# Kernel tuning notes

Measured on AMD Instinct MI355X. Metric: run time of the kernel, lower is better.

## Reference

```python
import jax, jax.numpy as jnp
import numpy as np

B, S, D_MODEL = 4, 1024, 1024
HEADS, D_KEY, D_VAL = 16, 64, 64


def setup_inputs() -> dict:
    key = jax.random.key(0)
    ks = jax.random.split(key, 8)
    # glorot-ish scaled params
    sk = 1.0 / np.sqrt(D_MODEL)
    X = jax.random.normal(ks[0], (B, S, D_MODEL), dtype=jnp.float32)
    Wk = jax.random.normal(ks[1], (HEADS, D_MODEL, D_KEY), dtype=jnp.float32) * sk
    Wq = jax.random.normal(ks[2], (HEADS, D_MODEL, D_KEY), dtype=jnp.float32) * sk
    Wv = jax.random.normal(ks[3], (HEADS, D_MODEL, D_VAL), dtype=jnp.float32) * sk
    bk = jnp.zeros((HEADS, D_KEY), dtype=jnp.float32)
    bq = jnp.zeros((HEADS, D_KEY), dtype=jnp.float32)
    bv = jnp.zeros((HEADS, D_VAL), dtype=jnp.float32)
    Wo = jax.random.normal(ks[4], (HEADS * D_VAL, D_MODEL), dtype=jnp.float32) * (1.0 / np.sqrt(HEADS * D_VAL))
    bo = jnp.zeros((D_MODEL,), dtype=jnp.float32)
    return {"X": X, "Wk": Wk, "bk": bk, "Wq": Wq, "bq": bq, "Wv": Wv, "bv": bv, "Wo": Wo, "bo": bo}


def reference(X, Wk, bk, Wq, bq, Wv, bv, Wo, bo):
    # Per-head projections, batched over heads (original loops in Python)
    K = jnp.einsum('bsd,hdk->bhsk', X, Wk) + bk[None, :, None, :]
    Q = jnp.einsum('bsd,hdk->bhsk', X, Wq) + bq[None, :, None, :]
    V = jnp.einsum('bsd,hdv->bhsv', X, Wv) + bv[None, :, None, :]
    d_k = K.shape[-1]
    scores = jnp.einsum('bhqk,bhsk->bhqs', Q, K) / jnp.sqrt(jnp.asarray(d_k, X.dtype))
    A = jax.nn.softmax(scores, axis=-1)           # [B,H,S,S]
    Z = jnp.einsum('bhqs,bhsv->bhqv', A, V)        # [B,H,S,Dv]
    # concat heads: [B,S,H*Dv]
    Zc = jnp.transpose(Z, (0, 2, 1, 3)).reshape(X.shape[0], X.shape[1], -1)
    # output projection + residual; dropout is identity at inference
    return Zc @ Wo + bo + X
```

## Files before the change

kernel.cpp:

```cpp
#include <hip/hip_runtime.h>
#include <hip/hip_bf16.h>

typedef __bf16 bf16x8 __attribute__((ext_vector_type(8)));
typedef float f32x4 __attribute__((ext_vector_type(4)));
typedef unsigned short u16;
typedef u16 u16x4 __attribute__((ext_vector_type(4)));
typedef u16 u16x8 __attribute__((ext_vector_type(8)));

#define LDA 72

__device__ inline u16 f2bf(float f) {
    union { float f; unsigned u; } v; v.f = f;
    unsigned r = v.u + 0x7fffu + ((v.u >> 16) & 1u);
    return (u16)(r >> 16);
}

#define GLD16(g, l) __builtin_amdgcn_global_load_lds( \
    (const __attribute__((address_space(1))) unsigned int*)(g), \
    (__attribute__((address_space(3))) unsigned int*)(l), 16, 0, 0)

__global__ void k_prep(const float* __restrict__ X, u16* __restrict__ Xb,
                       const float* __restrict__ Wk, const float* __restrict__ Wq,
                       const float* __restrict__ Wv, u16* __restrict__ WT,
                       const float* __restrict__ Wo, u16* __restrict__ WoT) {
    __shared__ u16 Ls[64 * LDA];
    int bid = blockIdx.x, t = threadIdx.x;
    if (bid < 4096) {
        int idx = bid * 256 + t;
        float4 v = *(const float4*)&X[(size_t)idx * 4];
        u16x4 o; o.x = f2bf(v.x); o.y = f2bf(v.y); o.z = f2bf(v.z); o.w = f2bf(v.w);
        *(u16x4*)&Xb[(size_t)idx * 4] = o;
        return;
    }
    if (bid < 4864) {
        int b2 = bid - 4096;
        int dt = b2 & 15, h = (b2 >> 4) & 15, p = b2 >> 8;
        const float* src = (p == 0 ? Wk : p == 1 ? Wq : Wv);
        int r0 = t >> 4, c4 = t & 15;
        for (int j = 0; j < 4; j++) {
            int d = r0 + j * 16;
            float4 v = *(const float4*)&src[((size_t)h * 1024 + dt * 64 + d) * 64 + c4 * 4];
            u16* q = &Ls[d * LDA + c4 * 4];
            q[0] = f2bf(v.x); q[1] = f2bf(v.y); q[2] = f2bf(v.z); q[3] = f2bf(v.w);
        }
        __syncthreads();
        int nk = t >> 2, cd = t & 3;
        u16 tmp[16];
        for (int j = 0; j < 16; j++) tmp[j] = Ls[(cd * 16 + j) * LDA + nk];
        size_t o = ((size_t)(p * 1024 + h * 64 + nk)) * 1024 + dt * 64 + cd * 16;
        *(u16x8*)&WT[o] = *(u16x8*)&tmp[0];
        *(u16x8*)&WT[o + 8] = *(u16x8*)&tmp[8];
        return;
    }
    {
        int b2 = bid - 4864;
        int dt = b2 & 15, nt2 = b2 >> 4;
        int r0 = t >> 4, c4 = t & 15;
        for (int j = 0; j < 4; j++) {
            int d = r0 + j * 16;
            float4 v = *(const float4*)&Wo[(size_t)(dt * 64 + d) * 1024 + nt2 * 64 + c4 * 4];
            u16* q = &Ls[d * LDA + c4 * 4];
            q[0] = f2bf(v.x); q[1] = f2bf(v.y); q[2] = f2bf(v.z); q[3] = f2bf(v.w);
        }
        __syncthreads();
        int nr = t >> 2, cd = t & 3;
        u16 tmp[16];
        for (int j = 0; j < 16; j++) tmp[j] = Ls[(cd * 16 + j) * LDA + nr];
        size_t o = ((size_t)(nt2 * 64 + nr)) * 1024 + dt * 64 + cd * 16;
        *(u16x8*)&WoT[o] = *(u16x8*)&tmp[0];
        *(u16x8*)&WoT[o + 8] = *(u16x8*)&tmp[8];
    }
}

__global__ __launch_bounds__(256) void k_qkv(
    const u16* __restrict__ Xb, const u16* __restrict__ WT,
    const float* __restrict__ bk, const float* __restrict__ bq, const float* __restrict__ bv,
    u16* __restrict__ Kw, u16* __restrict__ Qw, u16* __restrict__ Vtw)
{
    __shared__ u16 As[128 * 64];
    __shared__ u16 Bs[128 * 64];
    int tid = threadIdx.x, w = tid >> 6, lane = tid & 63, quad = lane >> 4, l16 = lane & 15;
    int wm = w & 1, wn = w >> 1;
    int m0 = blockIdx.x * 128, n0 = blockIdx.y * 128;
    int rl = lane >> 3, ch = lane & 7;
    int swch = ch ^ rl;
    const u16* Ag = Xb + (size_t)(m0 + w * 32 + rl) * 1024 + swch * 8;
    const u16* Bg = WT + (size_t)(n0 + w * 32 + rl) * 1024 + swch * 8;

    f32x4 acc[4][4] = {};
    for (int k0 = 0; k0 < 1024; k0 += 64) {
        for (int i = 0; i < 4; i++) {
            GLD16(Ag + (size_t)i * 8 * 1024 + k0, &As[(w * 32 + i * 8) * 64]);
            GLD16(Bg + (size_t)i * 8 * 1024 + k0, &Bs[(w * 32 + i * 8) * 64]);
        }
        __syncthreads();
        for (int ks = 0; ks < 2; ks++) {
            bf16x8 af[4], bf[4];
            int c = (ks << 2) | quad;
            for (int mt = 0; mt < 4; mt++) {
                int row = wm * 64 + mt * 16 + l16;
                af[mt] = *(bf16x8*)&As[row * 64 + (c ^ (row & 7)) * 8];
            }
            for (int nt = 0; nt < 4; nt++) {
                int row = wn * 64 + nt * 16 + l16;
                bf[nt] = *(bf16x8*)&Bs[row * 64 + (c ^ (row & 7)) * 8];
            }
            for (int mt = 0; mt < 4; mt++)
                for (int nt = 0; nt < 4; nt++)
                    acc[mt][nt] = __builtin_amdgcn_mfma_f32_16x16x32_bf16(af[mt], bf[nt], acc[mt][nt], 0, 0, 0);
        }
        __syncthreads();
    }
    int hb = blockIdx.y * 2 + wn;
    int p = hb >> 4, hh = hb & 15;
    const float* bias = (p == 0 ? bk : p == 1 ? bq : bv) + hh * 64;
    if (p < 2) {
        u16* dst = (p == 0) ? Kw : Qw;
        float sc = (p == 0) ? 0.125f : 1.0f;
        for (int mt = 0; mt < 4; mt++)
            for (int nt = 0; nt < 4; nt++) {
                int nk = nt * 16 + l16;
                float bb = bias[nk];
                for (int r = 0; r < 4; r++) {
                    int m = m0 + wm * 64 + mt * 16 + quad * 4 + r;
                    int b = m >> 10, s = m & 1023;
                    dst[((size_t)((b << 4) + hh) * 1024 + s) * 64 + nk] = f2bf((acc[mt][nt][r] + bb) * sc);
                }
            }
    } else {
        for (int mt = 0; mt < 4; mt++)
            for (int nt = 0; nt < 4; nt++) {
                int nk = nt * 16 + l16;
                float bb = bias[nk];
                int mb = m0 + wm * 64 + mt * 16 + quad * 4;
                int b = mb >> 10, s = mb & 1023;
                u16x4 o;
                for (int r = 0; r < 4; r++) o[r] = f2bf(acc[mt][nt][r] + bb);
                *(u16x4*)&Vtw[((size_t)((b << 4) + hh) * 64 + nk) * 1024 + s] = o;
            }
    }
}

__global__ __launch_bounds__(256) void k_attn(
    const u16* __restrict__ Qw, const u16* __restrict__ Kw,
    const u16* __restrict__ Vtw, u16* __restrict__ Zw)
{
    __shared__ u16 Ks[2][64 * 64];
    __shared__ u16 Vs[2][64 * 64];
    __shared__ u16 Ps[4 * 2 * 16 * LDA];
    int tid = threadIdx.x, w = tid >> 6, lane = tid & 63, quad = lane >> 4, l16 = lane & 15;
    int bh = blockIdx.x, q0 = blockIdx.y * 128;
    const u16* Qp = Qw + (size_t)bh * 65536;
    int rl = lane >> 3, ch = lane & 7, swch = ch ^ rl;
    const u16* Kg = Kw + (size_t)bh * 65536 + (w * 16 + rl) * 64 + swch * 8;
    const u16* Vg = Vtw + (size_t)bh * 65536 + (size_t)(w * 16 + rl) * 1024 + swch * 8;

    bf16x8 aq[2][2];
    for (int g = 0; g < 2; g++)
        for (int ks = 0; ks < 2; ks++)
            aq[g][ks] = *(const bf16x8*)&Qp[(size_t)(q0 + w * 32 + g * 16 + l16) * 64 + ks * 32 + quad * 8];

    f32x4 acc[2][4] = {};
    f32x4 accs[2] = {};
    __bf16 onev = (__bf16)1.0f;
    bf16x8 ones = {onev, onev, onev, onev, onev, onev, onev, onev};
    u16* Pw0 = Ps + (w * 2) * 16 * LDA;
    u16* Pw1 = Pw0 + 16 * LDA;

#define STAGE(st, buf) { int s0_ = (st) * 64; \
    for (int i = 0; i < 2; i++) { \
        GLD16(Kg + (s0_ + i * 8) * 64, &Ks[buf][(w * 16 + i * 8) * 64]); \
        GLD16(Vg + (size_t)i * 8 * 1024 + s0_, &Vs[buf][(w * 16 + i * 8) * 64]); } }

    STAGE(0, 0);
    for (int st = 0; st < 16; st++) {
        int buf = st & 1;
        __syncthreads();
        if (st < 15) STAGE(st + 1, buf ^ 1);
        f32x4 sacc[2][4] = {};
        for (int ks = 0; ks < 2; ks++) {
            int c = (ks << 2) | quad;
            for (int nt = 0; nt < 4; nt++) {
                int row = nt * 16 + l16;
                bf16x8 kf = *(bf16x8*)&Ks[buf][row * 64 + (c ^ (row & 7)) * 8];
                sacc[0][nt] = __builtin_amdgcn_mfma_f32_16x16x32_bf16(aq[0][ks], kf, sacc[0][nt], 0, 0, 0);
                sacc[1][nt] = __builtin_amdgcn_mfma_f32_16x16x32_bf16(aq[1][ks], kf, sacc[1][nt], 0, 0, 0);
            }
        }
        for (int g = 0; g < 2; g++) {
            u16* Pw = g ? Pw1 : Pw0;
            for (int nt = 0; nt < 4; nt++)
                for (int r = 0; r < 4; r++) {
                    float p = __builtin_exp2f(__builtin_fmaf(sacc[g][nt][r], 1.44269504f, -23.0831206f));
                    union { float f; unsigned u; } cv; cv.f = p;
                    Pw[(quad * 4 + r) * LDA + nt * 16 + l16] = (u16)((cv.u + 0x8000u) >> 16);
                }
        }
        for (int ks2 = 0; ks2 < 2; ks2++) {
            int c = (ks2 << 2) | quad;
            bf16x8 ap0 = *(bf16x8*)&Pw0[l16 * LDA + ks2 * 32 + quad * 8];
            bf16x8 ap1 = *(bf16x8*)&Pw1[l16 * LDA + ks2 * 32 + quad * 8];
            accs[0] = __builtin_amdgcn_mfma_f32_16x16x32_bf16(ap0, ones, accs[0], 0, 0, 0);
            accs[1] = __builtin_amdgcn_mfma_f32_16x16x32_bf16(ap1, ones, accs[1], 0, 0, 0);
            for (int ntv = 0; ntv < 4; ntv++) {
                int row = ntv * 16 + l16;
                bf16x8 vf = *(bf16x8*)&Vs[buf][row * 64 + (c ^ (row & 7)) * 8];
                acc[0][ntv] = __builtin_amdgcn_mfma_f32_16x16x32_bf16(ap0, vf, acc[0][ntv], 0, 0, 0);
                acc[1][ntv] = __builtin_amdgcn_mfma_f32_16x16x32_bf16(ap1, vf, acc[1][ntv], 0, 0, 0);
            }
        }
    }
#undef STAGE
    int b = bh >> 4, h = bh & 15;
    for (int g = 0; g < 2; g++)
        for (int r = 0; r < 4; r++) {
            float inv = 1.f / accs[g][r];
            int q = q0 + w * 32 + g * 16 + quad * 4 + r;
            for (int ntv = 0; ntv < 4; ntv++)
                Zw[((size_t)(b * 1024 + q)) * 1024 + h * 64 + ntv * 16 + l16] = f2bf(acc[g][ntv][r] * inv);
        }
}

__global__ __launch_bounds__(256) void k_oproj(
    const u16* __restrict__ Zw, const u16* __restrict__ WoT, const float* __restrict__ bo,
    const float* __restrict__ X, float* __restrict__ out)
{
    __shared__ u16 As[128 * 64];
    __shared__ u16 Bs[128 * 64];
    int tid = threadIdx.x, w = tid >> 6, lane = tid & 63, quad = lane >> 4, l16 = lane & 15;
    int wm = w & 1, wn = w >> 1;
    int m0 = blockIdx.x * 128, n0 = blockIdx.y * 128;
    int rl = lane >> 3, ch = lane & 7;
    int swch = ch ^ rl;
    const u16* Ag = Zw + (size_t)(m0 + w * 32 + rl) * 1024 + swch * 8;
    const u16* Bg = WoT + (size_t)(n0 + w * 32 + rl) * 1024 + swch * 8;

    f32x4 acc[4][4] = {};
    for (int k0 = 0; k0 < 1024; k0 += 64) {
        for (int i = 0; i < 4; i++) {
            GLD16(Ag + (size_t)i * 8 * 1024 + k0, &As[(w * 32 + i * 8) * 64]);
            GLD16(Bg + (size_t)i * 8 * 1024 + k0, &Bs[(w * 32 + i * 8) * 64]);
        }
        __syncthreads();
        for (int ks = 0; ks < 2; ks++) {
            bf16x8 af[4], bf[4];
            int c = (ks << 2) | quad;
            for (int mt = 0; mt < 4; mt++) {
                int row = wm * 64 + mt * 16 + l16;
                af[mt] = *(bf16x8*)&As[row * 64 + (c ^ (row & 7)) * 8];
            }
            for (int nt = 0; nt < 4; nt++) {
                int row = wn * 64 + nt * 16 + l16;
                bf[nt] = *(bf16x8*)&Bs[row * 64 + (c ^ (row & 7)) * 8];
            }
            for (int mt = 0; mt < 4; mt++)
                for (int nt = 0; nt < 4; nt++)
                    acc[mt][nt] = __builtin_amdgcn_mfma_f32_16x16x32_bf16(af[mt], bf[nt], acc[mt][nt], 0, 0, 0);
        }
        __syncthreads();
    }
    for (int mt = 0; mt < 4; mt++)
        for (int nt = 0; nt < 4; nt++) {
            int n = n0 + wn * 64 + nt * 16 + l16;
            float bb = bo[n];
            for (int r = 0; r < 4; r++) {
                int m = m0 + wm * 64 + mt * 16 + quad * 4 + r;
                out[(size_t)m * 1024 + n] = acc[mt][nt][r] + bb + X[(size_t)m * 1024 + n];
            }
        }
}

extern "C" void kernel_launch(void* const* d_in, const int* in_sizes, int n_in,
                              void* d_out, int out_size, void* d_ws, size_t ws_size,
                              hipStream_t stream) {
    const float* X  = (const float*)d_in[0];
    const float* Wk = (const float*)d_in[1];
    const float* bk = (const float*)d_in[2];
    const float* Wq = (const float*)d_in[3];
    const float* bq = (const float*)d_in[4];
    const float* Wv = (const float*)d_in[5];
    const float* bv = (const float*)d_in[6];
    const float* Wo = (const float*)d_in[7];
    const float* bo = (const float*)d_in[8];
    u16* ws = (u16*)d_ws;
    const size_t NQ = 4u * 16u * 1024u * 64u;
    u16* Qw  = ws;
    u16* Kw  = ws + NQ;
    u16* Vtw = ws + 2 * NQ;
    u16* Zw  = ws + 3 * NQ;
    u16* WT  = ws + 4 * NQ;
    u16* WoT = WT + 3 * 1048576;
    u16* Xb  = WoT + 1048576;
    float* outp = (float*)d_out;

    k_prep <<<5120, 256, 0, stream>>>(X, Xb, Wk, Wq, Wv, WT, Wo, WoT);
    k_qkv  <<<dim3(32, 24), 256, 0, stream>>>(Xb, WT, bk, bq, bv, Kw, Qw, Vtw);
    k_attn <<<dim3(64, 8), 256, 0, stream>>>(Qw, Kw, Vtw, Zw);
    k_oproj<<<dim3(32, 8), 256, 0, stream>>>(Zw, WoT, bo, X, outp);
}
```

Measured before the change: 187.6 us.

## Fuse all four stages into one persistent cooperative kernel with grid syncs

```diff
diff --git a/kernel.cpp b/kernel.cpp
--- a/kernel.cpp
+++ b/kernel.cpp
@@ -1,5 +1,8 @@
 #include <hip/hip_runtime.h>
 #include <hip/hip_bf16.h>
+#include <hip/hip_cooperative_groups.h>
+
+namespace cg = cooperative_groups;
 
 typedef __bf16 bf16x8 __attribute__((ext_vector_type(8)));
 typedef float f32x4 __attribute__((ext_vector_type(4)));
@@ -19,24 +22,21 @@
     (const __attribute__((address_space(1))) unsigned int*)(g), \
     (__attribute__((address_space(3))) unsigned int*)(l), 16, 0, 0)
 
-__global__ void k_prep(const float* __restrict__ X, u16* __restrict__ Xb,
-                       const float* __restrict__ Wk, const float* __restrict__ Wq,
-                       const float* __restrict__ Wv, u16* __restrict__ WT,
-                       const float* __restrict__ Wo, u16* __restrict__ WoT) {
-    __shared__ u16 Ls[64 * LDA];
-    int bid = blockIdx.x, t = threadIdx.x;
-    if (bid < 4096) {
-        int idx = bid * 256 + t;
+
+__device__ __forceinline__ void dev_prep(int u, int tid, u16* Ls,
+    const float* X, u16* Xb, const float* Wk, const float* Wq,
+    const float* Wv, u16* WT, const float* Wo, u16* WoT)
+{
+    if (u < 4096) {
+        int idx = u * 256 + tid;
         float4 v = *(const float4*)&X[(size_t)idx * 4];
         u16x4 o; o.x = f2bf(v.x); o.y = f2bf(v.y); o.z = f2bf(v.z); o.w = f2bf(v.w);
         *(u16x4*)&Xb[(size_t)idx * 4] = o;
-        return;
-    }
-    if (bid < 4864) {
-        int b2 = bid - 4096;
+    } else if (u < 4864) {
+        int b2 = u - 4096;
         int dt = b2 & 15, h = (b2 >> 4) & 15, p = b2 >> 8;
         const float* src = (p == 0 ? Wk : p == 1 ? Wq : Wv);
-        int r0 = t >> 4, c4 = t & 15;
+        int r0 = tid >> 4, c4 = tid & 15;
         for (int j = 0; j < 4; j++) {
             int d = r0 + j * 16;
             float4 v = *(const float4*)&src[((size_t)h * 1024 + dt * 64 + d) * 64 + c4 * 4];
@@ -44,18 +44,16 @@
             q[0] = f2bf(v.x); q[1] = f2bf(v.y); q[2] = f2bf(v.z); q[3] = f2bf(v.w);
         }
         __syncthreads();
-        int nk = t >> 2, cd = t & 3;
+        int nk = tid >> 2, cd = tid & 3;
         u16 tmp[16];
         for (int j = 0; j < 16; j++) tmp[j] = Ls[(cd * 16 + j) * LDA + nk];
         size_t o = ((size_t)(p * 1024 + h * 64 + nk)) * 1024 + dt * 64 + cd * 16;
         *(u16x8*)&WT[o] = *(u16x8*)&tmp[0];
         *(u16x8*)&WT[o + 8] = *(u16x8*)&tmp[8];
-        return;
-    }
-    {
-        int b2 = bid - 4864;
+    } else {
+        int b2 = u - 4864;
         int dt = b2 & 15, nt2 = b2 >> 4;
-        int r0 = t >> 4, c4 = t & 15;
+        int r0 = tid >> 4, c4 = tid & 15;
         for (int j = 0; j < 4; j++) {
             int d = r0 + j * 16;
             float4 v = *(const float4*)&Wo[(size_t)(dt * 64 + d) * 1024 + nt2 * 64 + c4 * 4];
@@ -63,7 +61,7 @@
             q[0] = f2bf(v.x); q[1] = f2bf(v.y); q[2] = f2bf(v.z); q[3] = f2bf(v.w);
         }
         __syncthreads();
-        int nr = t >> 2, cd = t & 3;
+        int nr = tid >> 2, cd = tid & 3;
         u16 tmp[16];
         for (int j = 0; j < 16; j++) tmp[j] = Ls[(cd * 16 + j) * LDA + nr];
         size_t o = ((size_t)(nt2 * 64 + nr)) * 1024 + dt * 64 + cd * 16;
@@ -72,18 +70,15 @@
     }
 }
 
-__global__ __launch_bounds__(256) void k_qkv(
-    const u16* __restrict__ Xb, const u16* __restrict__ WT,
-    const float* __restrict__ bk, const float* __restrict__ bq, const float* __restrict__ bv,
-    u16* __restrict__ Kw, u16* __restrict__ Qw, u16* __restrict__ Vtw)
-{
-    __shared__ u16 As[128 * 64];
-    __shared__ u16 Bs[128 * 64];
-    int tid = threadIdx.x, w = tid >> 6, lane = tid & 63, quad = lane >> 4, l16 = lane & 15;
+__device__ __forceinline__ void dev_qkv_tile(int m0, int nslice, int tid,
+    u16* As, u16* Bs, const u16* Xb, const u16* WT,
+    const float* bk, const float* bq, const float* bv,
+    u16* Kw, u16* Qw, u16* Vtw)
+{
+    int w = tid >> 6, lane = tid & 63, quad = lane >> 4, l16 = lane & 15;
     int wm = w & 1, wn = w >> 1;
-    int m0 = blockIdx.x * 128, n0 = blockIdx.y * 128;
-    int rl = lane >> 3, ch = lane & 7;
-    int swch = ch ^ rl;
+    int rl = lane >> 3, ch = lane & 7, swch = ch ^ rl;
+    int n0 = nslice * 128;
     const u16* Ag = Xb + (size_t)(m0 + w * 32 + rl) * 1024 + swch * 8;
     const u16* Bg = WT + (size_t)(n0 + w * 32 + rl) * 1024 + swch * 8;
 
@@ -111,7 +106,7 @@
         }
         __syncthreads();
     }
-    int hb = blockIdx.y * 2 + wn;
+    int hb = nslice * 2 + wn;
     int p = hb >> 4, hh = hb & 15;
     const float* bias = (p == 0 ? bk : p == 1 ? bq : bv) + hh * 64;
     if (p < 2) {
@@ -141,17 +136,13 @@
     }
 }
 
-__global__ __launch_bounds__(256) void k_attn(
-    const u16* __restrict__ Qw, const u16* __restrict__ Kw,
-    const u16* __restrict__ Vtw, u16* __restrict__ Zw)
-{
-    __shared__ u16 Ks[2][64 * 64];
-    __shared__ u16 Vs[2][64 * 64];
-    __shared__ u16 Ps[4 * 2 * 16 * LDA];
-    int tid = threadIdx.x, w = tid >> 6, lane = tid & 63, quad = lane >> 4, l16 = lane & 15;
-    int bh = blockIdx.x, q0 = blockIdx.y * 128;
+__device__ __forceinline__ void dev_attn(int bh, int q0, int tid,
+    u16* Ks, u16* Vs, u16* Ps,
+    const u16* Qw, const u16* Kw, const u16* Vtw, u16* Zw)
+{
+    int w = tid >> 6, lane = tid & 63, quad = lane >> 4, l16 = lane & 15;
+    int rl = lane >> 3, ch = lane & 7, swch = ch ^ rl;
     const u16* Qp = Qw + (size_t)bh * 65536;
-    int rl = lane >> 3, ch = lane & 7, swch = ch ^ rl;
     const u16* Kg = Kw + (size_t)bh * 65536 + (w * 16 + rl) * 64 + swch * 8;
     const u16* Vg = Vtw + (size_t)bh * 65536 + (size_t)(w * 16 + rl) * 1024 + swch * 8;
 
@@ -169,8 +160,8 @@
 
 #define STAGE(st, buf) { int s0_ = (st) * 64; \
     for (int i = 0; i < 2; i++) { \
-        GLD16(Kg + (s0_ + i * 8) * 64, &Ks[buf][(w * 16 + i * 8) * 64]); \
-        GLD16(Vg + (size_t)i * 8 * 1024 + s0_, &Vs[buf][(w * 16 + i * 8) * 64]); } }
+        GLD16(Kg + (s0_ + i * 8) * 64, Ks + (buf) * 4096 + (w * 16 + i * 8) * 64); \
+        GLD16(Vg + (size_t)i * 8 * 1024 + s0_, Vs + (buf) * 4096 + (w * 16 + i * 8) * 64); } }
 
     STAGE(0, 0);
     for (int st = 0; st < 16; st++) {
@@ -182,7 +173,7 @@
             int c = (ks << 2) | quad;
             for (int nt = 0; nt < 4; nt++) {
                 int row = nt * 16 + l16;
-                bf16x8 kf = *(bf16x8*)&Ks[buf][row * 64 + (c ^ (row & 7)) * 8];
+                bf16x8 kf = *(bf16x8*)&Ks[buf * 4096 + row * 64 + (c ^ (row & 7)) * 8];
                 sacc[0][nt] = __builtin_amdgcn_mfma_f32_16x16x32_bf16(aq[0][ks], kf, sacc[0][nt], 0, 0, 0);
                 sacc[1][nt] = __builtin_amdgcn_mfma_f32_16x16x32_bf16(aq[1][ks], kf, sacc[1][nt], 0, 0, 0);
             }
@@ -204,7 +195,7 @@
             accs[1] = __builtin_amdgcn_mfma_f32_16x16x32_bf16(ap1, ones, accs[1], 0, 0, 0);
             for (int ntv = 0; ntv < 4; ntv++) {
                 int row = ntv * 16 + l16;
-                bf16x8 vf = *(bf16x8*)&Vs[buf][row * 64 + (c ^ (row & 7)) * 8];
+                bf16x8 vf = *(bf16x8*)&Vs[buf * 4096 + row * 64 + (c ^ (row & 7)) * 8];
                 acc[0][ntv] = __builtin_amdgcn_mfma_f32_16x16x32_bf16(ap0, vf, acc[0][ntv], 0, 0, 0);
                 acc[1][ntv] = __builtin_amdgcn_mfma_f32_16x16x32_bf16(ap1, vf, acc[1][ntv], 0, 0, 0);
             }
@@ -221,53 +212,124 @@
         }
 }
 
-__global__ __launch_bounds__(256) void k_oproj(
-    const u16* __restrict__ Zw, const u16* __restrict__ WoT, const float* __restrict__ bo,
-    const float* __restrict__ X, float* __restrict__ out)
-{
-    __shared__ u16 As[128 * 64];
-    __shared__ u16 Bs[128 * 64];
-    int tid = threadIdx.x, w = tid >> 6, lane = tid & 63, quad = lane >> 4, l16 = lane & 15;
+__device__ __forceinline__ void dev_oproj_tile(int m0, int n0, int tid,
+    u16* As, u16* Bs, const u16* Zw, const u16* WoT,
+    const float* bo, const float* X, float* out)
+{
+    int w = tid >> 6, lane = tid & 63, quad = lane >> 4, l16 = lane & 15;
     int wm = w & 1, wn = w >> 1;
-    int m0 = blockIdx.x * 128, n0 = blockIdx.y * 128;
-    int rl = lane >> 3, ch = lane & 7;
-    int swch = ch ^ rl;
-    const u16* Ag = Zw + (size_t)(m0 + w * 32 + rl) * 1024 + swch * 8;
+    int rl = lane >> 3, ch = lane & 7, swch = ch ^ rl;
+    const u16* Ag = Zw + (size_t)(m0 + w * 16 + rl) * 1024 + swch * 8;
     const u16* Bg = WoT + (size_t)(n0 + w * 32 + rl) * 1024 + swch * 8;
 
-    f32x4 acc[4][4] = {};
+    f32x4 acc[2][4] = {};
     for (int k0 = 0; k0 < 1024; k0 += 64) {
-        for (int i = 0; i < 4; i++) {
-            GLD16(Ag + (size_t)i * 8 * 1024 + k0, &As[(w * 32 + i * 8) * 64]);
+        for (int i = 0; i < 2; i++)
+            GLD16(Ag + (size_t)i * 8 * 1024 + k0, &As[(w * 16 + i * 8) * 64]);
+        for (int i = 0; i < 4; i++)
             GLD16(Bg + (size_t)i * 8 * 1024 + k0, &Bs[(w * 32 + i * 8) * 64]);
-        }
         __syncthreads();
         for (int ks = 0; ks < 2; ks++) {
-            bf16x8 af[4], bf[4];
+            bf16x8 af[2], bf[4];
             int c = (ks << 2) | quad;
-            for (int mt = 0; mt < 4; mt++) {
-                int row = wm * 64 + mt * 16 + l16;
+            for (int mt = 0; mt < 2; mt++) {
+                int row = wm * 32 + mt * 16 + l16;
                 af[mt] = *(bf16x8*)&As[row * 64 + (c ^ (row & 7)) * 8];
             }
             for (int nt = 0; nt < 4; nt++) {
                 int row = wn * 64 + nt * 16 + l16;
                 bf[nt] = *(bf16x8*)&Bs[row * 64 + (c ^ (row & 7)) * 8];
             }
-            for (int mt = 0; mt < 4; mt++)
+            for (int mt = 0; mt < 2; mt++)
                 for (int nt = 0; nt < 4; nt++)
                     acc[mt][nt] = __builtin_amdgcn_mfma_f32_16x16x32_bf16(af[mt], bf[nt], acc[mt][nt], 0, 0, 0);
         }
         __syncthreads();
     }
-    for (int mt = 0; mt < 4; mt++)
+    for (int mt = 0; mt < 2; mt++)
         for (int nt = 0; nt < 4; nt++) {
             int n = n0 + wn * 64 + nt * 16 + l16;
             float bb = bo[n];
             for (int r = 0; r < 4; r++) {
-                int m = m0 + wm * 64 + mt * 16 + quad * 4 + r;
+                int m = m0 + wm * 32 + mt * 16 + quad * 4 + r;
                 out[(size_t)m * 1024 + n] = acc[mt][nt][r] + bb + X[(size_t)m * 1024 + n];
             }
         }
+}
+
+
+__global__ void k_prep(const float* __restrict__ X, u16* __restrict__ Xb,
+                       const float* __restrict__ Wk, const float* __restrict__ Wq,
+                       const float* __restrict__ Wv, u16* __restrict__ WT,
+                       const float* __restrict__ Wo, u16* __restrict__ WoT) {
+    __shared__ u16 Ls[64 * LDA];
+    dev_prep(blockIdx.x, threadIdx.x, Ls, X, Xb, Wk, Wq, Wv, WT, Wo, WoT);
+}
+
+__global__ __launch_bounds__(256) void k_qkv(
+    const u16* __restrict__ Xb, const u16* __restrict__ WT,
+    const float* __restrict__ bk, const float* __restrict__ bq, const float* __restrict__ bv,
+    u16* __restrict__ Kw, u16* __restrict__ Qw, u16* __restrict__ Vtw) {
+    __shared__ u16 As[128 * 64];
+    __shared__ u16 Bs[128 * 64];
+    dev_qkv_tile(blockIdx.x * 128, blockIdx.y, threadIdx.x, As, Bs,
+                 Xb, WT, bk, bq, bv, Kw, Qw, Vtw);
+}
+
+__global__ __launch_bounds__(256) void k_attn(
+    const u16* __restrict__ Qw, const u16* __restrict__ Kw,
+    const u16* __restrict__ Vtw, u16* __restrict__ Zw) {
+    __shared__ u16 Ks[2 * 64 * 64];
+    __shared__ u16 Vs[2 * 64 * 64];
+    __shared__ u16 Ps[4 * 2 * 16 * LDA];
+    dev_attn(blockIdx.x, blockIdx.y * 128, threadIdx.x, Ks, Vs, Ps, Qw, Kw, Vtw, Zw);
+}
+
+__global__ __launch_bounds__(256) void k_oproj(
+    const u16* __restrict__ Zw, const u16* __restrict__ WoT, const float* __restrict__ bo,
+    const float* __restrict__ X, float* __restrict__ out) {
+    __shared__ u16 As[64 * 64];
+    __shared__ u16 Bs[128 * 64];
+    dev_oproj_tile(blockIdx.x * 64, blockIdx.y * 128, threadIdx.x, As, Bs,
+                   Zw, WoT, bo, X, out);
+}
+
+__global__ __launch_bounds__(256, 2) void k_fused(
+    const float* __restrict__ X, const float* __restrict__ Wk,
+    const float* __restrict__ Wq, const float* __restrict__ Wv,
+    const float* __restrict__ Wo, const float* __restrict__ bk,
+    const float* __restrict__ bq, const float* __restrict__ bv,
+    const float* __restrict__ bo, u16* __restrict__ Xb,
+    u16* __restrict__ WT, u16* __restrict__ WoT,
+    u16* __restrict__ Kw, u16* __restrict__ Qw, u16* __restrict__ Vtw,
+    u16* __restrict__ Zw, float* __restrict__ out)
+{
+    __shared__ union SMem {
+        struct { u16 As[128 * 64]; u16 Bs[128 * 64]; } g;
+        struct { u16 Ks[2 * 64 * 64]; u16 Vs[2 * 64 * 64]; u16 Ps[4 * 2 * 16 * LDA]; } a;
+        struct { u16 As[64 * 64]; u16 Bs[128 * 64]; } o;
+        u16 Ls[64 * LDA];
+    } smem;
+    cg::grid_group grid = cg::this_grid();
+    int tid = threadIdx.x, blk = blockIdx.x;
+
+    for (int u = blk; u < 5120; u += 512) {
+        dev_prep(u, tid, smem.Ls, X, Xb, Wk, Wq, Wv, WT, Wo, WoT);
+        __syncthreads();
+    }
+    grid.sync();
+
+    for (int t = blk; t < 768; t += 512)
+        dev_qkv_tile((t & 31) * 128, t >> 5, tid, smem.g.As, smem.g.Bs,
+                     Xb, WT, bk, bq, bv, Kw, Qw, Vtw);
+    grid.sync();
+
+    dev_attn(blk & 63, (blk >> 6) * 128, tid, smem.a.Ks, smem.a.Vs, smem.a.Ps,
+             Qw, Kw, Vtw, Zw);
+    grid.sync();
+
+    dev_oproj_tile((blk & 63) * 64, (blk >> 6) * 128, tid, smem.o.As, smem.o.Bs,
+                   Zw, WoT, bo, X, out);
 }
 
 extern "C" void kernel_launch(void* const* d_in, const int* in_sizes, int n_in,
@@ -293,8 +355,22 @@
     u16* Xb  = WoT + 1048576;
     float* outp = (float*)d_out;
 
-    k_prep <<<5120, 256, 0, stream>>>(X, Xb, Wk, Wq, Wv, WT, Wo, WoT);
-    k_qkv  <<<dim3(32, 24), 256, 0, stream>>>(Xb, WT, bk, bq, bv, Kw, Qw, Vtw);
-    k_attn <<<dim3(64, 8), 256, 0, stream>>>(Qw, Kw, Vtw, Zw);
-    k_oproj<<<dim3(32, 8), 256, 0, stream>>>(Zw, WoT, bo, X, outp);
-}
+    int maxB = 0;
+    hipError_t qe = hipOccupancyMaxActiveBlocksPerMultiprocessor(
+        &maxB, (const void*)k_fused, 256, 0);
+    if (qe == hipSuccess && maxB >= 2) {
+        void* args[17] = {
+            (void*)&X, (void*)&Wk, (void*)&Wq, (void*)&Wv, (void*)&Wo,
+            (void*)&bk, (void*)&bq, (void*)&bv, (void*)&bo,
+            (void*)&Xb, (void*)&WT, (void*)&WoT,
+            (void*)&Kw, (void*)&Qw, (void*)&Vtw, (void*)&Zw, (void*)&outp
+        };
+        hipLaunchCooperativeKernel((const void*)k_fused, dim3(512), dim3(256),
+                                   args, 0, stream);
+    } else {
+        k_prep <<<5120, 256, 0, stream>>>(X, Xb, Wk, Wq, Wv, WT, Wo, WoT);
+        k_qkv  <<<dim3(32, 24), 256, 0, stream>>>(Xb, WT, bk, bq, bv, Kw, Qw, Vtw);
+        k_attn <<<dim3(64, 8), 256, 0, stream>>>(Qw, Kw, Vtw, Zw);
+        k_oproj<<<dim3(64, 8), 256, 0, stream>>>(Zw, WoT, bo, X, outp);
+    }
+}
```

Result: no change. 186.0 us (-0.8%).

## Shrink oproj M-tile for more blocks, transpose K/Q MFMA for vector stores

Applied to the files above, without the earlier changes.

```diff
diff --git a/kernel.cpp b/kernel.cpp
--- a/kernel.cpp
+++ b/kernel.cpp
@@ -24,19 +24,17 @@
                        const float* __restrict__ Wv, u16* __restrict__ WT,
                        const float* __restrict__ Wo, u16* __restrict__ WoT) {
     __shared__ u16 Ls[64 * LDA];
-    int bid = blockIdx.x, t = threadIdx.x;
-    if (bid < 4096) {
-        int idx = bid * 256 + t;
+    int u = blockIdx.x, tid = threadIdx.x;
+    if (u < 4096) {
+        int idx = u * 256 + tid;
         float4 v = *(const float4*)&X[(size_t)idx * 4];
         u16x4 o; o.x = f2bf(v.x); o.y = f2bf(v.y); o.z = f2bf(v.z); o.w = f2bf(v.w);
         *(u16x4*)&Xb[(size_t)idx * 4] = o;
-        return;
-    }
-    if (bid < 4864) {
-        int b2 = bid - 4096;
+    } else if (u < 4864) {
+        int b2 = u - 4096;
         int dt = b2 & 15, h = (b2 >> 4) & 15, p = b2 >> 8;
         const float* src = (p == 0 ? Wk : p == 1 ? Wq : Wv);
-        int r0 = t >> 4, c4 = t & 15;
+        int r0 = tid >> 4, c4 = tid & 15;
         for (int j = 0; j < 4; j++) {
             int d = r0 + j * 16;
             float4 v = *(const float4*)&src[((size_t)h * 1024 + dt * 64 + d) * 64 + c4 * 4];
@@ -44,18 +42,16 @@
             q[0] = f2bf(v.x); q[1] = f2bf(v.y); q[2] = f2bf(v.z); q[3] = f2bf(v.w);
         }
         __syncthreads();
-        int nk = t >> 2, cd = t & 3;
+        int nk = tid >> 2, cd = tid & 3;
         u16 tmp[16];
         for (int j = 0; j < 16; j++) tmp[j] = Ls[(cd * 16 + j) * LDA + nk];
         size_t o = ((size_t)(p * 1024 + h * 64 + nk)) * 1024 + dt * 64 + cd * 16;
         *(u16x8*)&WT[o] = *(u16x8*)&tmp[0];
         *(u16x8*)&WT[o + 8] = *(u16x8*)&tmp[8];
-        return;
-    }
-    {
-        int b2 = bid - 4864;
+    } else {
+        int b2 = u - 4864;
         int dt = b2 & 15, nt2 = b2 >> 4;
-        int r0 = t >> 4, c4 = t & 15;
+        int r0 = tid >> 4, c4 = tid & 15;
         for (int j = 0; j < 4; j++) {
             int d = r0 + j * 16;
             float4 v = *(const float4*)&Wo[(size_t)(dt * 64 + d) * 1024 + nt2 * 64 + c4 * 4];
@@ -63,7 +59,7 @@
             q[0] = f2bf(v.x); q[1] = f2bf(v.y); q[2] = f2bf(v.z); q[3] = f2bf(v.w);
         }
         __syncthreads();
-        int nr = t >> 2, cd = t & 3;
+        int nr = tid >> 2, cd = tid & 3;
         u16 tmp[16];
         for (int j = 0; j < 16; j++) tmp[j] = Ls[(cd * 16 + j) * LDA + nr];
         size_t o = ((size_t)(nt2 * 64 + nr)) * 1024 + dt * 64 + cd * 16;
@@ -72,7 +68,7 @@
     }
 }
 
-__global__ __launch_bounds__(256) void k_qkv(
+__global__ __launch_bounds__(256, 3) void k_qkv(
     const u16* __restrict__ Xb, const u16* __restrict__ WT,
     const float* __restrict__ bk, const float* __restrict__ bq, const float* __restrict__ bv,
     u16* __restrict__ Kw, u16* __restrict__ Qw, u16* __restrict__ Vtw)
@@ -82,10 +78,13 @@
     int tid = threadIdx.x, w = tid >> 6, lane = tid & 63, quad = lane >> 4, l16 = lane & 15;
     int wm = w & 1, wn = w >> 1;
     int m0 = blockIdx.x * 128, n0 = blockIdx.y * 128;
-    int rl = lane >> 3, ch = lane & 7;
-    int swch = ch ^ rl;
+    int rl = lane >> 3, ch = lane & 7, swch = ch ^ rl;
     const u16* Ag = Xb + (size_t)(m0 + w * 32 + rl) * 1024 + swch * 8;
     const u16* Bg = WT + (size_t)(n0 + w * 32 + rl) * 1024 + swch * 8;
+
+    int hb = blockIdx.y * 2 + wn;
+    int p = hb >> 4, hh = hb & 15;
+    bool ct = (p < 2);
 
     f32x4 acc[4][4] = {};
     for (int k0 = 0; k0 < 1024; k0 += 64) {
@@ -105,28 +104,36 @@
                 int row = wn * 64 + nt * 16 + l16;
                 bf[nt] = *(bf16x8*)&Bs[row * 64 + (c ^ (row & 7)) * 8];
             }
-            for (int mt = 0; mt < 4; mt++)
-                for (int nt = 0; nt < 4; nt++)
-                    acc[mt][nt] = __builtin_amdgcn_mfma_f32_16x16x32_bf16(af[mt], bf[nt], acc[mt][nt], 0, 0, 0);
-        }
-        __syncthreads();
-    }
-    int hb = blockIdx.y * 2 + wn;
-    int p = hb >> 4, hh = hb & 15;
+            if (ct) {
+                for (int mt = 0; mt < 4; mt++)
+                    for (int nt = 0; nt < 4; nt++)
+                        acc[mt][nt] = __builtin_amdgcn_mfma_f32_16x16x32_bf16(bf[nt], af[mt], acc[mt][nt], 0, 0, 0);
+            } else {
+                for (int mt = 0; mt < 4; mt++)
+                    for (int nt = 0; nt < 4; nt++)
+                        acc[mt][nt] = __builtin_amdgcn_mfma_f32_16x16x32_bf16(af[mt], bf[nt], acc[mt][nt], 0, 0, 0);
+            }
+        }
+        __syncthreads();
+    }
     const float* bias = (p == 0 ? bk : p == 1 ? bq : bv) + hh * 64;
-    if (p < 2) {
+    if (ct) {
         u16* dst = (p == 0) ? Kw : Qw;
         float sc = (p == 0) ? 0.125f : 1.0f;
-        for (int mt = 0; mt < 4; mt++)
-            for (int nt = 0; nt < 4; nt++) {
-                int nk = nt * 16 + l16;
-                float bb = bias[nk];
-                for (int r = 0; r < 4; r++) {
-                    int m = m0 + wm * 64 + mt * 16 + quad * 4 + r;
-                    int b = m >> 10, s = m & 1023;
-                    dst[((size_t)((b << 4) + hh) * 1024 + s) * 64 + nk] = f2bf((acc[mt][nt][r] + bb) * sc);
-                }
-            }
+        for (int mt = 0; mt < 4; mt++) {
+            int m = m0 + wm * 64 + mt * 16 + l16;
+            int b = m >> 10, s = m & 1023;
+            size_t base = ((size_t)((b << 4) + hh) * 1024 + s) * 64;
+            for (int nt = 0; nt < 4; nt++) {
+                float4 bb = *(const float4*)&bias[nt * 16 + quad * 4];
+                u16x4 o;
+                o[0] = f2bf((acc[mt][nt][0] + bb.x) * sc);
+                o[1] = f2bf((acc[mt][nt][1] + bb.y) * sc);
+                o[2] = f2bf((acc[mt][nt][2] + bb.z) * sc);
+                o[3] = f2bf((acc[mt][nt][3] + bb.w) * sc);
+                *(u16x4*)&dst[base + nt * 16 + quad * 4] = o;
+            }
+        }
     } else {
         for (int mt = 0; mt < 4; mt++)
             for (int nt = 0; nt < 4; nt++) {
@@ -225,46 +232,45 @@
     const u16* __restrict__ Zw, const u16* __restrict__ WoT, const float* __restrict__ bo,
     const float* __restrict__ X, float* __restrict__ out)
 {
-    __shared__ u16 As[128 * 64];
+    __shared__ u16 As[64 * 64];
     __shared__ u16 Bs[128 * 64];
     int tid = threadIdx.x, w = tid >> 6, lane = tid & 63, quad = lane >> 4, l16 = lane & 15;
     int wm = w & 1, wn = w >> 1;
-    int m0 = blockIdx.x * 128, n0 = blockIdx.y * 128;
-    int rl = lane >> 3, ch = lane & 7;
-    int swch = ch ^ rl;
-    const u16* Ag = Zw + (size_t)(m0 + w * 32 + rl) * 1024 + swch * 8;
+    int m0 = blockIdx.x * 64, n0 = blockIdx.y * 128;
+    int rl = lane >> 3, ch = lane & 7, swch = ch ^ rl;
+    const u16* Ag = Zw + (size_t)(m0 + w * 16 + rl) * 1024 + swch * 8;
     const u16* Bg = WoT + (size_t)(n0 + w * 32 + rl) * 1024 + swch * 8;
 
-    f32x4 acc[4][4] = {};
+    f32x4 acc[2][4] = {};
     for (int k0 = 0; k0 < 1024; k0 += 64) {
-        for (int i = 0; i < 4; i++) {
-            GLD16(Ag + (size_t)i * 8 * 1024 + k0, &As[(w * 32 + i * 8) * 64]);
+        for (int i = 0; i < 2; i++)
+            GLD16(Ag + (size_t)i * 8 * 1024 + k0, &As[(w * 16 + i * 8) * 64]);
+        for (int i = 0; i < 4; i++)
             GLD16(Bg + (size_t)i * 8 * 1024 + k0, &Bs[(w * 32 + i * 8) * 64]);
-        }
         __syncthreads();
         for (int ks = 0; ks < 2; ks++) {
-            bf16x8 af[4], bf[4];
+            bf16x8 af[2], bf[4];
             int c = (ks << 2) | quad;
-            for (int mt = 0; mt < 4; mt++) {
-                int row = wm * 64 + mt * 16 + l16;
+            for (int mt = 0; mt < 2; mt++) {
+                int row = wm * 32 + mt * 16 + l16;
                 af[mt] = *(bf16x8*)&As[row * 64 + (c ^ (row & 7)) * 8];
             }
             for (int nt = 0; nt < 4; nt++) {
                 int row = wn * 64 + nt * 16 + l16;
                 bf[nt] = *(bf16x8*)&Bs[row * 64 + (c ^ (row & 7)) * 8];
             }
-            for (int mt = 0; mt < 4; mt++)
+            for (int mt = 0; mt < 2; mt++)
                 for (int nt = 0; nt < 4; nt++)
                     acc[mt][nt] = __builtin_amdgcn_mfma_f32_16x16x32_bf16(af[mt], bf[nt], acc[mt][nt], 0, 0, 0);
         }
         __syncthreads();
     }
-    for (int mt = 0; mt < 4; mt++)
+    for (int mt = 0; mt < 2; mt++)
         for (int nt = 0; nt < 4; nt++) {
             int n = n0 + wn * 64 + nt * 16 + l16;
             float bb = bo[n];
             for (int r = 0; r < 4; r++) {
-                int m = m0 + wm * 64 + mt * 16 + quad * 4 + r;
+                int m = m0 + wm * 32 + mt * 16 + quad * 4 + r;
                 out[(size_t)m * 1024 + n] = acc[mt][nt][r] + bb + X[(size_t)m * 1024 + n];
             }
         }
@@ -296,5 +302,5 @@
     k_prep <<<5120, 256, 0, stream>>>(X, Xb, Wk, Wq, Wv, WT, Wo, WoT);
     k_qkv  <<<dim3(32, 24), 256, 0, stream>>>(Xb, WT, bk, bq, bv, Kw, Qw, Vtw);
     k_attn <<<dim3(64, 8), 256, 0, stream>>>(Qw, Kw, Vtw, Zw);
-    k_oproj<<<dim3(32, 8), 256, 0, stream>>>(Zw, WoT, bo, X, outp);
-}
+    k_oproj<<<dim3(64, 8), 256, 0, stream>>>(Zw, WoT, bo, X, outp);
+}
```

Result: no change. 186.0 us (-0.8%).
